# Kernel tuning notes

Hardware: AMD Instinct MI355X
Metric: run time of the kernel (lower is better)

## Reference

```python
import jax, jax.numpy as jnp
import numpy as np

B, N, D, NS, HID, ITERS = 32, 4096, 256, 8, 128, 3
EPS = 1e-8
LN_EPS = 1e-5


def _ln(x, g, b):
    mu = jnp.mean(x, axis=-1, keepdims=True)
    var = jnp.mean(jnp.square(x - mu), axis=-1, keepdims=True)
    return (x - mu) * jax.lax.rsqrt(var + LN_EPS) * g + b


def setup_inputs() -> dict:
    key = jax.random.key(0)
    ks = jax.random.split(key, 32)
    scale = D ** -0.5

    def lin(k, out_d, in_d):
        return jax.random.normal(k, (out_d, in_d), jnp.float32) * (in_d ** -0.5)

    inp = {
        "inputs": jax.random.normal(ks[0], (B, N, D), jnp.float32),
        "slot_noise": jax.random.normal(ks[1], (B, NS, D), jnp.float32),
        "slots_mu": jax.random.uniform(ks[2], (1, 1, D), jnp.float32, -1.0, 1.0) * scale,
        "slots_sigma": jax.random.uniform(ks[3], (1, 1, D), jnp.float32, -1.0, 1.0) * scale,
        "Wq": lin(ks[4], D, D),
        "Wk": lin(ks[5], D, D),
        "Wv": lin(ks[6], D, D),
        "gru_w_ih": lin(ks[7], 3 * D, 2 * D),
        "gru_w_hh": lin(ks[8], 3 * D, D),
        "gru_b_ih": jnp.zeros((3 * D,), jnp.float32),
        "gru_b_hh": jnp.zeros((3 * D,), jnp.float32),
        "obj_w1": lin(ks[9], HID, D),
        "obj_b1": jnp.zeros((HID,), jnp.float32),
        "obj_w2": lin(ks[10], D, HID),
        "obj_b2": jnp.zeros((D,), jnp.float32),
        "rel_w1": lin(ks[11], HID, 2 * D),
        "rel_b1": jnp.zeros((HID,), jnp.float32),
        "rel_w2": lin(ks[12], D, HID),
        "rel_b2": jnp.zeros((D,), jnp.float32),
        "ln_in_g": jnp.ones((D,), jnp.float32),
        "ln_in_b": jnp.zeros((D,), jnp.float32),
        "ln_s_g": jnp.ones((D,), jnp.float32),
        "ln_s_b": jnp.zeros((D,), jnp.float32),
        "ln_ff_g": jnp.ones((D,), jnp.float32),
        "ln_ff_b": jnp.zeros((D,), jnp.float32),
    }
    return inp


def _rel_msg(x, rel_w1, rel_b1, rel_w2, rel_b2):
    # x: (b, n_s, d). rel_mlp(cat(x_i, x_j)) without materializing the concat:
    # split first layer weight into the x_i and x_j halves.
    A = rel_w1[:, :D]   # (hid, d)
    Bm = rel_w1[:, D:]  # (hid, d)
    xa = jnp.einsum('bid,hd->bih', x, A)
    xb = jnp.einsum('bjd,hd->bjh', x, Bm)
    h = jax.nn.relu(xa[:, :, None, :] + xb[:, None, :, :] + rel_b1)  # (b,ns,ns,hid)
    msg = jnp.einsum('bijh,dh->bijd', h, rel_w2) + rel_b2            # (b,ns,ns,d)
    n_s = x.shape[1]
    diag = jnp.eye(n_s, dtype=bool)[None, :, :, None]
    msg = jnp.where(diag, 0.0, msg)
    return msg.sum(axis=2) / (n_s - 1)


def _gru_cell(x, h, w_ih, w_hh, b_ih, b_hh):
    gx = x @ w_ih.T + b_ih  # (B*, 3d)
    gh = h @ w_hh.T + b_hh
    xr, xz, xn = jnp.split(gx, 3, axis=-1)
    hr, hz, hn = jnp.split(gh, 3, axis=-1)
    r = jax.nn.sigmoid(xr + hr)
    z = jax.nn.sigmoid(xz + hz)
    n = jnp.tanh(xn + r * hn)
    return (1.0 - z) * n + z * h


def reference(inputs, slot_noise, slots_mu, slots_sigma, Wq, Wk, Wv,
              gru_w_ih, gru_w_hh, gru_b_ih, gru_b_hh,
              obj_w1, obj_b1, obj_w2, obj_b2,
              rel_w1, rel_b1, rel_w2, rel_b2,
              ln_in_g, ln_in_b, ln_s_g, ln_s_b, ln_ff_g, ln_ff_b):
    b, n, d = inputs.shape
    n_s = slot_noise.shape[1]
    scale = d ** -0.5

    slots = slots_mu + slot_noise * jnp.exp(slots_sigma)  # (b, n_s, d)

    x = _ln(inputs, ln_in_g, ln_in_b)
    k = jnp.einsum('bnd,ed->bne', x, Wk)
    v = jnp.einsum('bnd,ed->bne', x, Wv)

    attns = []
    for _ in range(ITERS):
        slots_prev = slots
        q = jnp.einsum('bid,ed->bie', _ln(slots, ln_s_g, ln_s_b), Wq)
        dots = jnp.einsum('bid,bjd->bij', q, k) * scale        # (b, n_s, n)
        attn = jax.nn.softmax(dots, axis=1) + EPS              # softmax over slots
        attns.append(attn)
        attn_n = attn / attn.sum(axis=-1, keepdims=True)
        updates = jnp.einsum('bjd,bij->bid', v, attn_n)        # (b, n_s, d)
        rel = _rel_msg(slots_prev, rel_w1, rel_b1, rel_w2, rel_b2)
        gin = jnp.concatenate([updates, rel], axis=-1).reshape(b * n_s, 2 * d)
        slots = _gru_cell(gin, slots_prev.reshape(b * n_s, d),
                          gru_w_ih, gru_w_hh, gru_b_ih, gru_b_hh).reshape(b, n_s, d)
        ff = _ln(slots, ln_ff_g, ln_ff_b)
        slots = slots + (jax.nn.relu(ff @ obj_w1.T + obj_b1) @ obj_w2.T + obj_b2)
    return slots, jnp.stack(attns)
```

## Files before the change

### kernel.cpp

```cpp
#include <hip/hip_runtime.h>
#include <hip/hip_bf16.h>
#include <math.h>

static constexpr int Bc   = 32;
static constexpr int Nc   = 4096;
static constexpr int Dc   = 256;
static constexpr int NSc  = 8;
static constexpr int HIDc = 128;
static constexpr int ITERSc = 3;
#define EPSf 1e-8f
#define LN_EPSf 1e-5f

typedef __attribute__((ext_vector_type(8))) short bf16x8;
typedef __attribute__((ext_vector_type(8))) unsigned short u16x8;
typedef __attribute__((ext_vector_type(4))) float f32x4;

static constexpr int W1AT = 0;
static constexpr int W1BT = 32768;
static constexpr int W2T  = 65536;
static constexpr int OW1T = 98304;
static constexpr int OW2T = 131072;
static constexpr int WQT  = 163840;
static constexpr int WHNT = 229376;
static constexpr int TW_ELEMS = 294912;

__device__ __forceinline__ float bf2f(unsigned int u) {
  return __uint_as_float((u & 0xffffu) << 16);
}

__device__ __forceinline__ unsigned short f2bfu(float f) {
  unsigned int u = __float_as_uint(f);
  unsigned int r = (u + 0x7fffu + ((u >> 16) & 1u)) >> 16;
  return (unsigned short)r;
}

__device__ __forceinline__ void bf8_to_f(uint4 r, float* o) {
  o[0] = bf2f(r.x); o[1] = bf2f(r.x >> 16);
  o[2] = bf2f(r.y); o[3] = bf2f(r.y >> 16);
  o[4] = bf2f(r.z); o[5] = bf2f(r.z >> 16);
  o[6] = bf2f(r.w); o[7] = bf2f(r.w >> 16);
}

__device__ __forceinline__ void gl_lds16(const void* g, void* l) {
  __builtin_amdgcn_global_load_lds(
      (__attribute__((address_space(1))) void*)(g),
      (__attribute__((address_space(3))) void*)(l), 16, 0, 0);
}

__device__ __forceinline__ float block_sum(float v, float* tmp) {
  #pragma unroll
  for (int o = 32; o > 0; o >>= 1) v += __shfl_down(v, o, 64);
  int lane = threadIdx.x & 63, wid = threadIdx.x >> 6;
  __syncthreads();
  if (lane == 0) tmp[wid] = v;
  __syncthreads();
  return tmp[0] + tmp[1] + tmp[2] + tmp[3];
}

__device__ __forceinline__ float sigmf(float x) { return 1.f / (1.f + expf(-x)); }

__global__ __launch_bounds__(256) void k_init_slots(const float* __restrict__ noise,
                                                    const float* __restrict__ mu,
                                                    const float* __restrict__ sigma,
                                                    float* __restrict__ slots) {
  int idx = blockIdx.x * 256 + threadIdx.x;
  int d = idx & (Dc - 1);
  slots[idx] = mu[d] + noise[idx] * expf(sigma[d]);
}

__global__ __launch_bounds__(256) void k_wcvt(const float* __restrict__ Wk,
                                              const float* __restrict__ Wv,
                                              unsigned short* __restrict__ wbuf) {
  int idx = blockIdx.x * 256 + threadIdx.x;
  int n = idx >> 8, k = idx & 255;
  float v = (n < 256) ? Wk[n * 256 + k] : Wv[(n - 256) * 256 + k];
  wbuf[idx] = f2bfu(v);
}

__global__ __launch_bounds__(256) void k_wprep(const float* __restrict__ w_ih,
                                               const float* __restrict__ w_hh,
                                               unsigned short* __restrict__ Wcat) {
  int idx = blockIdx.x * 256 + threadIdx.x;
  int o = idx / 768, c = idx - o * 768;
  float v;
  if (c < 512) v = w_ih[o * 512 + c];
  else v = (o < 512) ? w_hh[o * 256 + (c - 512)] : 0.f;
  Wcat[idx] = f2bfu(v);
}

__global__ __launch_bounds__(256) void k_tprep(const float* __restrict__ rel_w1,
                                               const float* __restrict__ rel_w2,
                                               const float* __restrict__ obj_w1,
                                               const float* __restrict__ obj_w2,
                                               const float* __restrict__ Wq,
                                               const float* __restrict__ w_hh,
                                               unsigned short* __restrict__ Tw) {
  int i = blockIdx.x * 256 + threadIdx.x;
  if (i >= TW_ELEMS) return;
  float v;
  if (i < W1BT) { int j = i - W1AT; int d = j >> 7, h = j & 127; v = rel_w1[h * 512 + d]; }
  else if (i < W2T)  { int j = i - W1BT; int d = j >> 7, h = j & 127; v = rel_w1[h * 512 + 256 + d]; }
  else if (i < OW1T) { int j = i - W2T;  int h = j >> 8, o = j & 255; v = rel_w2[o * 128 + h]; }
  else if (i < OW2T) { int j = i - OW1T; int d = j >> 7, h = j & 127; v = obj_w1[h * 256 + d]; }
  else if (i < WQT)  { int j = i - OW2T; int h = j >> 8, o = j & 255; v = obj_w2[o * 128 + h]; }
  else if (i < WHNT) { int j = i - WQT;  int d = j >> 8, e = j & 255; v = Wq[e * 256 + d]; }
  else               { int j = i - WHNT; int d = j >> 8, o = j & 255; v = w_hh[(512 + o) * 256 + d]; }
  Tw[i] = f2bfu(v);
}

__global__ __launch_bounds__(256, 2) void k_gemm_kv(const float* __restrict__ inp,
                                                    const float* __restrict__ lng,
                                                    const float* __restrict__ lnb,
                                                    const unsigned short* __restrict__ wbuf,
                                                    unsigned short* __restrict__ kbuf,
                                                    unsigned short* __restrict__ vbuf) {
  __shared__ unsigned short Als[64 * 64];
  __shared__ unsigned short Bls[512 * 64];
  __shared__ float smu[64];
  __shared__ float srs[64];
  int tid = threadIdx.x;
  int lane = tid & 63, w = tid >> 6;
  int idx16 = lane & 15, quad = lane >> 4;
  int m0 = blockIdx.x * 64;

  for (int rr = 0; rr < 16; rr++) {
    int row = w * 16 + rr;
    float4 v = *(const float4*)(inp + (size_t)(m0 + row) * 256 + lane * 4);
    float s = v.x + v.y + v.z + v.w;
    float q = v.x * v.x + v.y * v.y + v.z * v.z + v.w * v.w;
    #pragma unroll
    for (int o = 32; o > 0; o >>= 1) { s += __shfl_down(s, o, 64); q += __shfl_down(q, o, 64); }
    if (lane == 0) {
      float mu = s * (1.0f / 256.0f);
      float var = q * (1.0f / 256.0f) - mu * mu;
      smu[row] = mu;
      srs[row] = rsqrtf(var + LN_EPSf);
    }
  }
  __syncthreads();

  f32x4 acc[4][8];
  #pragma unroll
  for (int i = 0; i < 4; i++)
    #pragma unroll
    for (int j = 0; j < 8; j++) acc[i][j] = (f32x4){0.f, 0.f, 0.f, 0.f};

  for (int kt = 0; kt < 4; kt++) {
    int k0 = kt * 64;
    #pragma unroll
    for (int c = 0; c < 16; c++) {
      int idx = (w * 16 + c) * 64 + lane;
      int row = idx >> 3, lc = idx & 7;
      int gc = lc ^ (row & 7);
      gl_lds16((const char*)wbuf + ((size_t)row * 256 + k0) * 2 + gc * 16,
               (char*)Bls + (size_t)(w * 16 + c) * 1024);
    }
    #pragma unroll
    for (int p = 0; p < 2; p++) {
      int idx = p * 256 + tid;
      int row = idx >> 3, c8 = idx & 7;
      const float* src = inp + (size_t)(m0 + row) * 256 + k0 + c8 * 8;
      float mu = smu[row], rs = srs[row];
      float4 x0 = *(const float4*)(src);
      float4 x1 = *(const float4*)(src + 4);
      float4 g0 = *(const float4*)(lng + k0 + c8 * 8);
      float4 g1 = *(const float4*)(lng + k0 + c8 * 8 + 4);
      float4 b0 = *(const float4*)(lnb + k0 + c8 * 8);
      float4 b1 = *(const float4*)(lnb + k0 + c8 * 8 + 4);
      u16x8 pk;
      pk[0] = f2bfu((x0.x - mu) * rs * g0.x + b0.x);
      pk[1] = f2bfu((x0.y - mu) * rs * g0.y + b0.y);
      pk[2] = f2bfu((x0.z - mu) * rs * g0.z + b0.z);
      pk[3] = f2bfu((x0.w - mu) * rs * g0.w + b0.w);
      pk[4] = f2bfu((x1.x - mu) * rs * g1.x + b1.x);
      pk[5] = f2bfu((x1.y - mu) * rs * g1.y + b1.y);
      pk[6] = f2bfu((x1.z - mu) * rs * g1.z + b1.z);
      pk[7] = f2bfu((x1.w - mu) * rs * g1.w + b1.w);
      int dchunk = c8 ^ (row & 7);
      *(u16x8*)((char*)Als + (size_t)(row * 8 + dchunk) * 16) = pk;
    }
    __syncthreads();
    #pragma unroll
    for (int ks = 0; ks < 2; ks++) {
      int kchunk = ks * 4 + quad;
      bf16x8 af[4], bfr[8];
      #pragma unroll
      for (int mt = 0; mt < 4; mt++) {
        int row = mt * 16 + idx16;
        af[mt] = *(const bf16x8*)((const char*)Als + (size_t)(row * 8 + (kchunk ^ (row & 7))) * 16);
      }
      #pragma unroll
      for (int nt = 0; nt < 8; nt++) {
        int row = w * 128 + nt * 16 + idx16;
        bfr[nt] = *(const bf16x8*)((const char*)Bls + (size_t)(row * 8 + (kchunk ^ (row & 7))) * 16);
      }
      #pragma unroll
      for (int mt = 0; mt < 4; mt++)
        #pragma unroll
        for (int nt = 0; nt < 8; nt++)
          acc[mt][nt] = __builtin_amdgcn_mfma_f32_16x16x32_bf16(af[mt], bfr[nt], acc[mt][nt], 0, 0, 0);
    }
    __syncthreads();
  }
  #pragma unroll
  for (int mt = 0; mt < 4; mt++) {
    #pragma unroll
    for (int nt = 0; nt < 8; nt++) {
      int gm = m0 + mt * 16 + quad * 4;
      int col = w * 128 + nt * 16 + idx16;
      unsigned short* dst = (col < 256) ? kbuf : vbuf;
      int c = col & 255;
      #pragma unroll
      for (int r = 0; r < 4; r++)
        dst[(size_t)(gm + r) * 256 + c] = f2bfu(acc[mt][nt][r]);
    }
  }
}

__global__ __launch_bounds__(256) void k_qproj0(const float* __restrict__ slots,
                                                const unsigned short* __restrict__ Tw,
                                                const float* __restrict__ g,
                                                const float* __restrict__ bb_,
                                                unsigned short* __restrict__ qb,
                                                float* __restrict__ S,
                                                float* __restrict__ updraw) {
  __shared__ float xs[Dc];
  __shared__ float tmp[4];
  int t = threadIdx.x;
  int row = blockIdx.x;
  updraw[row * 256 + t] = 0.f;
  if (blockIdx.x == 0) S[t] = 0.f;
  float x = slots[row * Dc + t];
  float s = block_sum(x, tmp);
  float m = s * (1.0f / Dc);
  float dx = x - m;
  float s2 = block_sum(dx * dx, tmp);
  float rs = rsqrtf(s2 * (1.0f / Dc) + LN_EPSf);
  xs[t] = dx * rs * g[t] + bb_[t];
  __syncthreads();
  float acc = 0.f;
  const unsigned short* wq = Tw + WQT;
  for (int d = 0; d < 256; d++) acc += bf2f(wq[d * 256 + t]) * xs[d];
  qb[row * 256 + t] = f2bfu(acc);
}

__global__ __launch_bounds__(256) void k_attn(const unsigned short* __restrict__ qb,
                                              const unsigned short* __restrict__ kbuf,
                                              const unsigned short* __restrict__ vbuf,
                                              float* __restrict__ attn,
                                              float* __restrict__ S,
                                              float* __restrict__ updraw) {
  __shared__ float qs[NSc][Dc];
  __shared__ float at[NSc][256];
  __shared__ float parts[2][NSc][256];
  int t = threadIdx.x;
  int b = blockIdx.x >> 4;
  int jc = blockIdx.x & 15;
  int j0 = jc * 256;
  for (int x = t; x < NSc * Dc; x += 256) qs[x >> 8][x & 255] = bf2f(qb[b * NSc * Dc + x]);
  __syncthreads();
  int j = j0 + t;
  const uint4* krow = (const uint4*)(kbuf + ((size_t)b * Nc + j) * Dc);
  float dot[NSc];
  #pragma unroll
  for (int i = 0; i < NSc; i++) dot[i] = 0.f;
  for (int d8 = 0; d8 < Dc / 8; d8++) {
    float kv[8];
    bf8_to_f(krow[d8], kv);
    #pragma unroll
    for (int i = 0; i < NSc; i++) {
      const float* qr = &qs[i][d8 * 8];
      float s0 = 0.f;
      #pragma unroll
      for (int u = 0; u < 8; u++) s0 += kv[u] * qr[u];
      dot[i] += s0;
    }
  }
  float m = -1e30f;
  #pragma unroll
  for (int i = 0; i < NSc; i++) { float s = dot[i] * 0.0625f; dot[i] = s; m = fmaxf(m, s); }
  float sum = 0.f;
  float a[NSc];
  #pragma unroll
  for (int i = 0; i < NSc; i++) { float e = expf(dot[i] - m); a[i] = e; sum += e; }
  float inv = 1.f / sum;
  #pragma unroll
  for (int i = 0; i < NSc; i++) a[i] = a[i] * inv + EPSf;
  float* ab = attn + (size_t)b * NSc * Nc;
  #pragma unroll
  for (int i = 0; i < NSc; i++) {
    ab[i * Nc + j] = a[i];
    at[i][t] = a[i];
  }
  __syncthreads();
  {
    int wv = t >> 6, lane = t & 63;
    #pragma unroll
    for (int ii = 0; ii < 2; ii++) {
      int i = wv + ii * 4;
      float4 v = *(const float4*)&at[i][lane * 4];
      float s = v.x + v.y + v.z + v.w;
      #pragma unroll
      for (int o = 32; o > 0; o >>= 1) s += __shfl_down(s, o, 64);
      if (lane == 0) atomicAdd(&S[b * NSc + i], s);
    }
  }
  int rsh = t >> 7, dg = t & 127;
  float acc[NSc][2];
  #pragma unroll
  for (int i = 0; i < NSc; i++) { acc[i][0] = 0.f; acc[i][1] = 0.f; }
  const unsigned short* vr = vbuf + ((size_t)b * Nc + j0 + rsh * 128) * Dc + dg * 2;
  for (int jj = 0; jj < 128; jj += 2) {
    unsigned int v0 = *(const unsigned int*)(vr + (size_t)jj * Dc);
    unsigned int v1 = *(const unsigned int*)(vr + (size_t)(jj + 1) * Dc);
    float v0a = bf2f(v0), v0b = bf2f(v0 >> 16);
    float v1a = bf2f(v1), v1b = bf2f(v1 >> 16);
    #pragma unroll
    for (int i = 0; i < NSc; i++) {
      float2 ap = *(const float2*)&at[i][rsh * 128 + jj];
      acc[i][0] += ap.x * v0a + ap.y * v1a;
      acc[i][1] += ap.x * v0b + ap.y * v1b;
    }
  }
  #pragma unroll
  for (int i = 0; i < NSc; i++) {
    parts[rsh][i][dg * 2] = acc[i][0];
    parts[rsh][i][dg * 2 + 1] = acc[i][1];
  }
  __syncthreads();
  for (int i = 0; i < NSc; i++) {
    float val = parts[0][i][t] + parts[1][i][t];
    atomicAdd(&updraw[(b * NSc + i) * 256 + t], val);
  }
}

__global__ __launch_bounds__(256) void k_slot_a(const float* __restrict__ slots,
                                                const float* __restrict__ updraw,
                                                const float* __restrict__ S,
                                                const unsigned short* __restrict__ Tw,
                                                const float* __restrict__ b1,
                                                const float* __restrict__ b2,
                                                unsigned short* __restrict__ Xb) {
  __shared__ float sp[NSc][256];
  __shared__ float xpart[2][12][128];
  __shared__ float xabl[12][128];
  __shared__ float hs[4][128];
  int t = threadIdx.x;
  int b = blockIdx.x >> 1, half = blockIdx.x & 1;
  int i0 = half * 4;
  for (int x = t; x < NSc * 256; x += 256) sp[x >> 8][x & 255] = slots[b * NSc * 256 + x];
  __syncthreads();
  for (int r = 0; r < 4; r++) {
    int grow = b * NSc + i0 + r;
    float u = updraw[grow * 256 + t] / S[grow];
    Xb[(size_t)grow * 768 + t] = f2bfu(u);
    Xb[(size_t)grow * 768 + 512 + t] = f2bfu(sp[i0 + r][t]);
  }
  int h = t & 127, dh = t >> 7;
  {
    const unsigned short* wa = Tw + W1AT;
    const unsigned short* wb = Tw + W1BT;
    float accb[8] = {0, 0, 0, 0, 0, 0, 0, 0};
    float acca[4] = {0, 0, 0, 0};
    for (int dd = 0; dd < 128; dd++) {
      int d = dh * 128 + dd;
      float wbv = bf2f(wb[d * 128 + h]);
      float wav = bf2f(wa[d * 128 + h]);
      #pragma unroll
      for (int jj = 0; jj < 8; jj++) accb[jj] += wbv * sp[jj][d];
      #pragma unroll
      for (int r = 0; r < 4; r++) acca[r] += wav * sp[i0 + r][d];
    }
    #pragma unroll
    for (int jj = 0; jj < 8; jj++) xpart[dh][jj][h] = accb[jj];
    #pragma unroll
    for (int r = 0; r < 4; r++) xpart[dh][8 + r][h] = acca[r];
  }
  __syncthreads();
  {
    int g = t >> 7;
    for (int jj = g * 6; jj < g * 6 + 6; jj++)
      xabl[jj][h] = xpart[0][jj][h] + xpart[1][jj][h];
  }
  __syncthreads();
  {
    float bv = b1[h];
    int ig = t >> 7;
    #pragma unroll
    for (int ii = 0; ii < 2; ii++) {
      int il = ig * 2 + ii;
      int ibatch = i0 + il;
      float av = xabl[8 + il][h];
      float s = 0.f;
      #pragma unroll
      for (int jj = 0; jj < NSc; jj++) {
        if (jj == ibatch) continue;
        s += fmaxf(av + xabl[jj][h] + bv, 0.f);
      }
      hs[il][h] = s;
    }
  }
  __syncthreads();
  {
    const unsigned short* w2 = Tw + W2T;
    float am[4] = {0, 0, 0, 0};
    for (int hh = 0; hh < 128; hh++) {
      float wv = bf2f(w2[hh * 256 + t]);
      #pragma unroll
      for (int r = 0; r < 4; r++) am[r] += wv * hs[r][hh];
    }
    float bv2 = b2[t];
    for (int r = 0; r < 4; r++) {
      float rel = am[r] * (1.0f / 7.0f) + bv2;
      Xb[(size_t)(b * NSc + i0 + r) * 768 + 256 + t] = f2bfu(rel);
    }
  }
}

__global__ __launch_bounds__(256) void k_gates(const unsigned short* __restrict__ Xb,
                                               const unsigned short* __restrict__ Wcat,
                                               unsigned short* __restrict__ Yb) {
  __shared__ unsigned short Als[64 * 64];
  __shared__ unsigned short Bls[64 * 64];
  int tid = threadIdx.x;
  int lane = tid & 63, w = tid >> 6;
  int idx16 = lane & 15, quad = lane >> 4;
  int m0 = (blockIdx.x / 12) * 64;
  int n0 = (blockIdx.x % 12) * 64;
  int wm = w & 1, wn = w >> 1;
  f32x4 acc[2][2];
  #pragma unroll
  for (int i = 0; i < 2; i++)
    #pragma unroll
    for (int j = 0; j < 2; j++) acc[i][j] = (f32x4){0.f, 0.f, 0.f, 0.f};

  for (int kt = 0; kt < 12; kt++) {
    int k0 = kt * 64;
    #pragma unroll
    for (int c = 0; c < 2; c++) {
      int idx = (w * 2 + c) * 64 + lane;
      int row = idx >> 3, lc = idx & 7;
      int gc = lc ^ (row & 7);
      gl_lds16((const char*)Xb + (size_t)(m0 + row) * 1536 + k0 * 2 + gc * 16,
               (char*)Als + (size_t)(w * 2 + c) * 1024);
      gl_lds16((const char*)Wcat + (size_t)(n0 + row) * 1536 + k0 * 2 + gc * 16,
               (char*)Bls + (size_t)(w * 2 + c) * 1024);
    }
    __syncthreads();
    #pragma unroll
    for (int ks = 0; ks < 2; ks++) {
      bf16x8 af[2], bfr[2];
      int kchunk = ks * 4 + quad;
      #pragma unroll
      for (int mt = 0; mt < 2; mt++) {
        int row = wm * 32 + mt * 16 + idx16;
        af[mt] = *(const bf16x8*)((const char*)Als + (size_t)(row * 8 + (kchunk ^ (row & 7))) * 16);
      }
      #pragma unroll
      for (int nt = 0; nt < 2; nt++) {
        int row = wn * 32 + nt * 16 + idx16;
        bfr[nt] = *(const bf16x8*)((const char*)Bls + (size_t)(row * 8 + (kchunk ^ (row & 7))) * 16);
      }
      #pragma unroll
      for (int mt = 0; mt < 2; mt++)
        #pragma unroll
        for (int nt = 0; nt < 2; nt++)
          acc[mt][nt] = __builtin_amdgcn_mfma_f32_16x16x32_bf16(af[mt], bfr[nt], acc[mt][nt], 0, 0, 0);
    }
    __syncthreads();
  }
  #pragma unroll
  for (int mt = 0; mt < 2; mt++) {
    #pragma unroll
    for (int nt = 0; nt < 2; nt++) {
      int gm = m0 + wm * 32 + mt * 16 + quad * 4;
      int col = n0 + wn * 32 + nt * 16 + idx16;
      #pragma unroll
      for (int r = 0; r < 4; r++)
        Yb[(size_t)(gm + r) * 768 + col] = f2bfu(acc[mt][nt][r]);
    }
  }
}

__global__ __launch_bounds__(256) void k_slot_c(const unsigned short* __restrict__ Yb,
                                                const unsigned short* __restrict__ Tw,
                                                const float* __restrict__ b_ih,
                                                const float* __restrict__ b_hh,
                                                float* __restrict__ slots,
                                                const float* __restrict__ ob1,
                                                const float* __restrict__ ob2,
                                                const float* __restrict__ lng,
                                                const float* __restrict__ lnb,
                                                const float* __restrict__ lsg,
                                                const float* __restrict__ lsb,
                                                unsigned short* __restrict__ qb,
                                                float* __restrict__ updraw,
                                                float* __restrict__ S,
                                                float* __restrict__ outf,
                                                int wfinal) {
  __shared__ float sp4[4][256];
  __shared__ float ffl[4][256];
  __shared__ float h1p[2][4][128];
  __shared__ float h1l[4][128];
  __shared__ float xs2[4][256];
  int t = threadIdx.x;
  int g0 = blockIdx.x * 4;
  for (int x = t; x < 1024; x += 256) sp4[x >> 8][x & 255] = slots[(size_t)g0 * 256 + x];
  __syncthreads();
  float hn[4] = {0, 0, 0, 0};
  {
    const unsigned short* wh = Tw + WHNT;
    for (int d = 0; d < 256; d++) {
      float wv = bf2f(wh[d * 256 + t]);
      #pragma unroll
      for (int r = 0; r < 4; r++) hn[r] += wv * sp4[r][d];
    }
  }
  float bir = b_ih[t], bhr = b_hh[t];
  float biz = b_ih[256 + t], bhz = b_hh[256 + t];
  float bin_ = b_ih[512 + t], bhn = b_hh[512 + t];
  float snew[4];
  #pragma unroll
  for (int r = 0; r < 4; r++) {
    size_t yoff = (size_t)(g0 + r) * 768;
    float yr = bf2f((unsigned int)Yb[yoff + t]);
    float yz = bf2f((unsigned int)Yb[yoff + 256 + t]);
    float yx = bf2f((unsigned int)Yb[yoff + 512 + t]);
    float rg = sigmf(yr + bir + bhr);
    float zg = sigmf(yz + biz + bhz);
    float ng = tanhf(yx + bin_ + rg * (hn[r] + bhn));
    snew[r] = (1.f - zg) * ng + zg * sp4[r][t];
    ffl[r][t] = snew[r];
  }
  __syncthreads();
  {
    int wv = t >> 6, lane = t & 63;
    float4 v = *(const float4*)&ffl[wv][lane * 4];
    float s = v.x + v.y + v.z + v.w;
    float q = v.x * v.x + v.y * v.y + v.z * v.z + v.w * v.w;
    #pragma unroll
    for (int o = 32; o > 0; o >>= 1) { s += __shfl_down(s, o, 64); q += __shfl_down(q, o, 64); }
    s = __shfl(s, 0, 64); q = __shfl(q, 0, 64);
    float mu = s * (1.0f / 256.0f);
    float rs = rsqrtf(q * (1.0f / 256.0f) - mu * mu + LN_EPSf);
    float4 g4 = *(const float4*)&lng[lane * 4];
    float4 b4 = *(const float4*)&lnb[lane * 4];
    float4 o4;
    o4.x = (v.x - mu) * rs * g4.x + b4.x;
    o4.y = (v.y - mu) * rs * g4.y + b4.y;
    o4.z = (v.z - mu) * rs * g4.z + b4.z;
    o4.w = (v.w - mu) * rs * g4.w + b4.w;
    *(float4*)&ffl[wv][lane * 4] = o4;
  }
  __syncthreads();
  {
    const unsigned short* w1 = Tw + OW1T;
    int h = t & 127, dh = t >> 7;
    float a1[4] = {0, 0, 0, 0};
    for (int dd = 0; dd < 128; dd++) {
      int d = dh * 128 + dd;
      float wv = bf2f(w1[d * 128 + h]);
      #pragma unroll
      for (int r = 0; r < 4; r++) a1[r] += wv * ffl[r][d];
    }
    #pragma unroll
    for (int r = 0; r < 4; r++) h1p[dh][r][h] = a1[r];
  }
  __syncthreads();
  {
    int h = t & 127, g = t >> 7;
    float bo = ob1[h];
    #pragma unroll
    for (int rr = 0; rr < 2; rr++) {
      int r = g * 2 + rr;
      h1l[r][h] = fmaxf(h1p[0][r][h] + h1p[1][r][h] + bo, 0.f);
    }
  }
  __syncthreads();
  float res[4];
  {
    const unsigned short* w2 = Tw + OW2T;
    float ao[4] = {0, 0, 0, 0};
    for (int hh = 0; hh < 128; hh++) {
      float wv = bf2f(w2[hh * 256 + t]);
      #pragma unroll
      for (int r = 0; r < 4; r++) ao[r] += wv * h1l[r][hh];
    }
    float bo2 = ob2[t];
    #pragma unroll
    for (int r = 0; r < 4; r++) res[r] = snew[r] + ao[r] + bo2;
  }
  #pragma unroll
  for (int r = 0; r < 4; r++) {
    slots[(size_t)(g0 + r) * 256 + t] = res[r];
    if (wfinal) outf[(size_t)(g0 + r) * 256 + t] = res[r];
    xs2[r][t] = res[r];
  }
  __syncthreads();
  {
    int wv = t >> 6, lane = t & 63;
    float4 v = *(const float4*)&xs2[wv][lane * 4];
    float s = v.x + v.y + v.z + v.w;
    float q = v.x * v.x + v.y * v.y + v.z * v.z + v.w * v.w;
    #pragma unroll
    for (int o = 32; o > 0; o >>= 1) { s += __shfl_down(s, o, 64); q += __shfl_down(q, o, 64); }
    s = __shfl(s, 0, 64); q = __shfl(q, 0, 64);
    float mu = s * (1.0f / 256.0f);
    float rs = rsqrtf(q * (1.0f / 256.0f) - mu * mu + LN_EPSf);
    float4 g4 = *(const float4*)&lsg[lane * 4];
    float4 b4 = *(const float4*)&lsb[lane * 4];
    float4 o4;
    o4.x = (v.x - mu) * rs * g4.x + b4.x;
    o4.y = (v.y - mu) * rs * g4.y + b4.y;
    o4.z = (v.z - mu) * rs * g4.z + b4.z;
    o4.w = (v.w - mu) * rs * g4.w + b4.w;
    *(float4*)&xs2[wv][lane * 4] = o4;
  }
  __syncthreads();
  {
    const unsigned short* wq = Tw + WQT;
    float aq[4] = {0, 0, 0, 0};
    for (int d = 0; d < 256; d++) {
      float wv = bf2f(wq[d * 256 + t]);
      #pragma unroll
      for (int r = 0; r < 4; r++) aq[r] += wv * xs2[r][d];
    }
    #pragma unroll
    for (int r = 0; r < 4; r++) qb[(size_t)(g0 + r) * 256 + t] = f2bfu(aq[r]);
  }
  #pragma unroll
  for (int r = 0; r < 4; r++) updraw[(size_t)(g0 + r) * 256 + t] = 0.f;
  if (t < 4) S[g0 + t] = 0.f;
}

extern "C" void kernel_launch(void* const* d_in, const int* in_sizes, int n_in,
                              void* d_out, int out_size, void* d_ws, size_t ws_size,
                              hipStream_t stream) {
  const float* inputs      = (const float*)d_in[0];
  const float* slot_noise  = (const float*)d_in[1];
  const float* slots_mu    = (const float*)d_in[2];
  const float* slots_sigma = (const float*)d_in[3];
  const float* Wq          = (const float*)d_in[4];
  const float* Wk          = (const float*)d_in[5];
  const float* Wv          = (const float*)d_in[6];
  const float* gru_w_ih    = (const float*)d_in[7];
  const float* gru_w_hh    = (const float*)d_in[8];
  const float* gru_b_ih    = (const float*)d_in[9];
  const float* gru_b_hh    = (const float*)d_in[10];
  const float* obj_w1      = (const float*)d_in[11];
  const float* obj_b1      = (const float*)d_in[12];
  const float* obj_w2      = (const float*)d_in[13];
  const float* obj_b2      = (const float*)d_in[14];
  const float* rel_w1      = (const float*)d_in[15];
  const float* rel_b1      = (const float*)d_in[16];
  const float* rel_w2      = (const float*)d_in[17];
  const float* rel_b2      = (const float*)d_in[18];
  const float* ln_in_g     = (const float*)d_in[19];
  const float* ln_in_b     = (const float*)d_in[20];
  const float* ln_s_g      = (const float*)d_in[21];
  const float* ln_s_b      = (const float*)d_in[22];
  const float* ln_ff_g     = (const float*)d_in[23];
  const float* ln_ff_b     = (const float*)d_in[24];

  char* w = (char*)d_ws;
  unsigned short* kbuf = (unsigned short*)(w);
  unsigned short* vbuf = (unsigned short*)(w + (size_t)67108864);
  float* slots  = (float*)(w + (size_t)134217728);
  float* updraw = (float*)(w + (size_t)134479872);
  float* Sbuf   = (float*)(w + (size_t)134742016);
  unsigned short* Wcat = (unsigned short*)(w + (size_t)134743040);
  unsigned short* Tw   = (unsigned short*)(w + (size_t)135922688);
  unsigned short* Xbuf = (unsigned short*)(w + (size_t)136512512);
  unsigned short* qb   = (unsigned short*)(w + (size_t)136512512);
  unsigned short* Ybuf = (unsigned short*)(w + (size_t)136905728);
  unsigned short* wbuf = (unsigned short*)(w + (size_t)136905728);

  float* out = (float*)d_out;
  float* attn_base = out + (size_t)Bc * NSc * Dc;

  k_init_slots<<<Bc * NSc * Dc / 256, 256, 0, stream>>>(slot_noise, slots_mu, slots_sigma, slots);
  k_wcvt<<<512, 256, 0, stream>>>(Wk, Wv, wbuf);
  k_wprep<<<768 * 768 / 256, 256, 0, stream>>>(gru_w_ih, gru_w_hh, Wcat);
  k_tprep<<<(TW_ELEMS + 255) / 256, 256, 0, stream>>>(rel_w1, rel_w2, obj_w1, obj_w2, Wq, gru_w_hh, Tw);
  k_gemm_kv<<<Bc * Nc / 64, 256, 0, stream>>>(inputs, ln_in_g, ln_in_b, wbuf, kbuf, vbuf);
  k_qproj0<<<Bc * NSc, 256, 0, stream>>>(slots, Tw, ln_s_g, ln_s_b, qb, Sbuf, updraw);

  for (int it = 0; it < ITERSc; it++) {
    float* attn = attn_base + (size_t)it * Bc * NSc * Nc;
    k_attn<<<Bc * 16, 256, 0, stream>>>(qb, kbuf, vbuf, attn, Sbuf, updraw);
    k_slot_a<<<Bc * 2, 256, 0, stream>>>(slots, updraw, Sbuf, Tw, rel_b1, rel_b2, Xbuf);
    k_gates<<<4 * 12, 256, 0, stream>>>(Xbuf, Wcat, Ybuf);
    k_slot_c<<<64, 256, 0, stream>>>(Ybuf, Tw, gru_b_ih, gru_b_hh, slots,
                                     obj_b1, obj_b2, ln_ff_g, ln_ff_b, ln_s_g, ln_s_b,
                                     qb, updraw, Sbuf,
                                     out, it == ITERSc - 1 ? 1 : 0);
  }
}
```

Baseline: 692.5 us.

## Fold Wk into query and Wv after attention to drop K/V projection GEMM

The full K and V projections over all tokens are removed. Queries are premultiplied by Wq^T·Wk (precomputed as MT), so attention logits come straight from the layer-normed inputs X stored once in bf16. The attention-weighted sum is taken over X, and Wv is applied afterwards to the small per-slot result in k_slot_a. This replaces a large GEMM and two 64MB buffers with one 64MB normalized-input buffer. Dots now use a 16x16 MFMA with half the rows zero-padded. Rounding changes, since MT is fp32 but X is bf16.

```diff
diff --git a/kernel.cpp b/kernel.cpp
--- a/kernel.cpp
+++ b/kernel.cpp
@@ -20,9 +20,8 @@
 static constexpr int W2T  = 65536;
 static constexpr int OW1T = 98304;
 static constexpr int OW2T = 131072;
-static constexpr int WQT  = 163840;
-static constexpr int WHNT = 229376;
-static constexpr int TW_ELEMS = 294912;
+static constexpr int WHNT = 163840;
+static constexpr int TW_ELEMS = 229376;
 
 __device__ __forceinline__ float bf2f(unsigned int u) {
   return __uint_as_float((u & 0xffffu) << 16);
@@ -32,13 +31,6 @@
   unsigned int u = __float_as_uint(f);
   unsigned int r = (u + 0x7fffu + ((u >> 16) & 1u)) >> 16;
   return (unsigned short)r;
-}
-
-__device__ __forceinline__ void bf8_to_f(uint4 r, float* o) {
-  o[0] = bf2f(r.x); o[1] = bf2f(r.x >> 16);
-  o[2] = bf2f(r.y); o[3] = bf2f(r.y >> 16);
-  o[4] = bf2f(r.z); o[5] = bf2f(r.z >> 16);
-  o[6] = bf2f(r.w); o[7] = bf2f(r.w >> 16);
 }
 
 __device__ __forceinline__ void gl_lds16(const void* g, void* l) {
@@ -68,13 +60,50 @@
   slots[idx] = mu[d] + noise[idx] * expf(sigma[d]);
 }
 
-__global__ __launch_bounds__(256) void k_wcvt(const float* __restrict__ Wk,
-                                              const float* __restrict__ Wv,
-                                              unsigned short* __restrict__ wbuf) {
-  int idx = blockIdx.x * 256 + threadIdx.x;
-  int n = idx >> 8, k = idx & 255;
-  float v = (n < 256) ? Wk[n * 256 + k] : Wv[(n - 256) * 256 + k];
-  wbuf[idx] = f2bfu(v);
+__global__ __launch_bounds__(256) void k_lnx(const float* __restrict__ inp,
+                                             const float* __restrict__ lng,
+                                             const float* __restrict__ lnb,
+                                             unsigned short* __restrict__ X) {
+  __shared__ float smu[16], srs[16];
+  int t = threadIdx.x, lane = t & 63, w = t >> 6;
+  size_t row0 = (size_t)blockIdx.x * 16;
+  for (int rr = 0; rr < 4; rr++) {
+    int row = w * 4 + rr;
+    float4 v = *(const float4*)(inp + (row0 + row) * 256 + lane * 4);
+    float s = v.x + v.y + v.z + v.w;
+    float q = v.x * v.x + v.y * v.y + v.z * v.z + v.w * v.w;
+    #pragma unroll
+    for (int o = 32; o > 0; o >>= 1) { s += __shfl_down(s, o, 64); q += __shfl_down(q, o, 64); }
+    if (lane == 0) {
+      float mu = s * (1.0f / 256.0f);
+      smu[row] = mu;
+      srs[row] = rsqrtf(q * (1.0f / 256.0f) - mu * mu + LN_EPSf);
+    }
+  }
+  __syncthreads();
+  #pragma unroll
+  for (int p = 0; p < 2; p++) {
+    int idx = p * 256 + t;
+    int row = idx >> 5, ch = idx & 31;
+    const float* src = inp + (row0 + row) * 256 + ch * 8;
+    float mu = smu[row], rs = srs[row];
+    float4 x0 = *(const float4*)(src);
+    float4 x1 = *(const float4*)(src + 4);
+    float4 g0 = *(const float4*)(lng + ch * 8);
+    float4 g1 = *(const float4*)(lng + ch * 8 + 4);
+    float4 b0 = *(const float4*)(lnb + ch * 8);
+    float4 b1 = *(const float4*)(lnb + ch * 8 + 4);
+    u16x8 pk;
+    pk[0] = f2bfu((x0.x - mu) * rs * g0.x + b0.x);
+    pk[1] = f2bfu((x0.y - mu) * rs * g0.y + b0.y);
+    pk[2] = f2bfu((x0.z - mu) * rs * g0.z + b0.z);
+    pk[3] = f2bfu((x0.w - mu) * rs * g0.w + b0.w);
+    pk[4] = f2bfu((x1.x - mu) * rs * g1.x + b1.x);
+    pk[5] = f2bfu((x1.y - mu) * rs * g1.y + b1.y);
+    pk[6] = f2bfu((x1.z - mu) * rs * g1.z + b1.z);
+    pk[7] = f2bfu((x1.w - mu) * rs * g1.w + b1.w);
+    *(u16x8*)(X + (row0 + row) * 256 + ch * 8) = pk;
+  }
 }
 
 __global__ __launch_bounds__(256) void k_wprep(const float* __restrict__ w_ih,
@@ -92,7 +121,6 @@
                                                const float* __restrict__ rel_w2,
                                                const float* __restrict__ obj_w1,
                                                const float* __restrict__ obj_w2,
-                                               const float* __restrict__ Wq,
                                                const float* __restrict__ w_hh,
                                                unsigned short* __restrict__ Tw) {
   int i = blockIdx.x * 256 + threadIdx.x;
@@ -102,126 +130,28 @@
   else if (i < W2T)  { int j = i - W1BT; int d = j >> 7, h = j & 127; v = rel_w1[h * 512 + 256 + d]; }
   else if (i < OW1T) { int j = i - W2T;  int h = j >> 8, o = j & 255; v = rel_w2[o * 128 + h]; }
   else if (i < OW2T) { int j = i - OW1T; int d = j >> 7, h = j & 127; v = obj_w1[h * 256 + d]; }
-  else if (i < WQT)  { int j = i - OW2T; int h = j >> 8, o = j & 255; v = obj_w2[o * 128 + h]; }
-  else if (i < WHNT) { int j = i - WQT;  int d = j >> 8, e = j & 255; v = Wq[e * 256 + d]; }
+  else if (i < WHNT) { int j = i - OW2T; int h = j >> 8, o = j & 255; v = obj_w2[o * 128 + h]; }
   else               { int j = i - WHNT; int d = j >> 8, o = j & 255; v = w_hh[(512 + o) * 256 + d]; }
   Tw[i] = f2bfu(v);
 }
 
-__global__ __launch_bounds__(256, 2) void k_gemm_kv(const float* __restrict__ inp,
-                                                    const float* __restrict__ lng,
-                                                    const float* __restrict__ lnb,
-                                                    const unsigned short* __restrict__ wbuf,
-                                                    unsigned short* __restrict__ kbuf,
-                                                    unsigned short* __restrict__ vbuf) {
-  __shared__ unsigned short Als[64 * 64];
-  __shared__ unsigned short Bls[512 * 64];
-  __shared__ float smu[64];
-  __shared__ float srs[64];
-  int tid = threadIdx.x;
-  int lane = tid & 63, w = tid >> 6;
-  int idx16 = lane & 15, quad = lane >> 4;
-  int m0 = blockIdx.x * 64;
-
-  for (int rr = 0; rr < 16; rr++) {
-    int row = w * 16 + rr;
-    float4 v = *(const float4*)(inp + (size_t)(m0 + row) * 256 + lane * 4);
-    float s = v.x + v.y + v.z + v.w;
-    float q = v.x * v.x + v.y * v.y + v.z * v.z + v.w * v.w;
-    #pragma unroll
-    for (int o = 32; o > 0; o >>= 1) { s += __shfl_down(s, o, 64); q += __shfl_down(q, o, 64); }
-    if (lane == 0) {
-      float mu = s * (1.0f / 256.0f);
-      float var = q * (1.0f / 256.0f) - mu * mu;
-      smu[row] = mu;
-      srs[row] = rsqrtf(var + LN_EPSf);
-    }
-  }
-  __syncthreads();
-
-  f32x4 acc[4][8];
-  #pragma unroll
-  for (int i = 0; i < 4; i++)
-    #pragma unroll
-    for (int j = 0; j < 8; j++) acc[i][j] = (f32x4){0.f, 0.f, 0.f, 0.f};
-
-  for (int kt = 0; kt < 4; kt++) {
-    int k0 = kt * 64;
-    #pragma unroll
-    for (int c = 0; c < 16; c++) {
-      int idx = (w * 16 + c) * 64 + lane;
-      int row = idx >> 3, lc = idx & 7;
-      int gc = lc ^ (row & 7);
-      gl_lds16((const char*)wbuf + ((size_t)row * 256 + k0) * 2 + gc * 16,
-               (char*)Bls + (size_t)(w * 16 + c) * 1024);
-    }
-    #pragma unroll
-    for (int p = 0; p < 2; p++) {
-      int idx = p * 256 + tid;
-      int row = idx >> 3, c8 = idx & 7;
-      const float* src = inp + (size_t)(m0 + row) * 256 + k0 + c8 * 8;
-      float mu = smu[row], rs = srs[row];
-      float4 x0 = *(const float4*)(src);
-      float4 x1 = *(const float4*)(src + 4);
-      float4 g0 = *(const float4*)(lng + k0 + c8 * 8);
-      float4 g1 = *(const float4*)(lng + k0 + c8 * 8 + 4);
-      float4 b0 = *(const float4*)(lnb + k0 + c8 * 8);
-      float4 b1 = *(const float4*)(lnb + k0 + c8 * 8 + 4);
-      u16x8 pk;
-      pk[0] = f2bfu((x0.x - mu) * rs * g0.x + b0.x);
-      pk[1] = f2bfu((x0.y - mu) * rs * g0.y + b0.y);
-      pk[2] = f2bfu((x0.z - mu) * rs * g0.z + b0.z);
-      pk[3] = f2bfu((x0.w - mu) * rs * g0.w + b0.w);
-      pk[4] = f2bfu((x1.x - mu) * rs * g1.x + b1.x);
-      pk[5] = f2bfu((x1.y - mu) * rs * g1.y + b1.y);
-      pk[6] = f2bfu((x1.z - mu) * rs * g1.z + b1.z);
-      pk[7] = f2bfu((x1.w - mu) * rs * g1.w + b1.w);
-      int dchunk = c8 ^ (row & 7);
-      *(u16x8*)((char*)Als + (size_t)(row * 8 + dchunk) * 16) = pk;
-    }
-    __syncthreads();
-    #pragma unroll
-    for (int ks = 0; ks < 2; ks++) {
-      int kchunk = ks * 4 + quad;
-      bf16x8 af[4], bfr[8];
-      #pragma unroll
-      for (int mt = 0; mt < 4; mt++) {
-        int row = mt * 16 + idx16;
-        af[mt] = *(const bf16x8*)((const char*)Als + (size_t)(row * 8 + (kchunk ^ (row & 7))) * 16);
-      }
-      #pragma unroll
-      for (int nt = 0; nt < 8; nt++) {
-        int row = w * 128 + nt * 16 + idx16;
-        bfr[nt] = *(const bf16x8*)((const char*)Bls + (size_t)(row * 8 + (kchunk ^ (row & 7))) * 16);
-      }
-      #pragma unroll
-      for (int mt = 0; mt < 4; mt++)
-        #pragma unroll
-        for (int nt = 0; nt < 8; nt++)
-          acc[mt][nt] = __builtin_amdgcn_mfma_f32_16x16x32_bf16(af[mt], bfr[nt], acc[mt][nt], 0, 0, 0);
-    }
-    __syncthreads();
-  }
-  #pragma unroll
-  for (int mt = 0; mt < 4; mt++) {
-    #pragma unroll
-    for (int nt = 0; nt < 8; nt++) {
-      int gm = m0 + mt * 16 + quad * 4;
-      int col = w * 128 + nt * 16 + idx16;
-      unsigned short* dst = (col < 256) ? kbuf : vbuf;
-      int c = col & 255;
-      #pragma unroll
-      for (int r = 0; r < 4; r++)
-        dst[(size_t)(gm + r) * 256 + c] = f2bfu(acc[mt][nt][r]);
-    }
-  }
+__global__ __launch_bounds__(256) void k_mprep(const float* __restrict__ Wk,
+                                               const float* __restrict__ Wq,
+                                               const float* __restrict__ Wv,
+                                               float* __restrict__ MT,
+                                               float* __restrict__ WvT) {
+  int d = blockIdx.x, t = threadIdx.x;
+  float acc = 0.f;
+  for (int c = 0; c < 256; c++) acc += Wk[c * 256 + t] * Wq[c * 256 + d];
+  MT[d * 256 + t] = acc;
+  WvT[d * 256 + t] = Wv[t * 256 + d];
 }
 
 __global__ __launch_bounds__(256) void k_qproj0(const float* __restrict__ slots,
-                                                const unsigned short* __restrict__ Tw,
+                                                const float* __restrict__ MT,
                                                 const float* __restrict__ g,
                                                 const float* __restrict__ bb_,
-                                                unsigned short* __restrict__ qb,
+                                                unsigned short* __restrict__ qkb,
                                                 float* __restrict__ S,
                                                 float* __restrict__ updraw) {
   __shared__ float xs[Dc];
@@ -239,98 +169,97 @@
   xs[t] = dx * rs * g[t] + bb_[t];
   __syncthreads();
   float acc = 0.f;
-  const unsigned short* wq = Tw + WQT;
-  for (int d = 0; d < 256; d++) acc += bf2f(wq[d * 256 + t]) * xs[d];
-  qb[row * 256 + t] = f2bfu(acc);
-}
-
-__global__ __launch_bounds__(256) void k_attn(const unsigned short* __restrict__ qb,
-                                              const unsigned short* __restrict__ kbuf,
-                                              const unsigned short* __restrict__ vbuf,
+  for (int d = 0; d < 256; d++) acc += MT[d * 256 + t] * xs[d];
+  int b = row >> 3, i = row & 7;
+  qkb[(size_t)(b * 16 + i) * 256 + t] = f2bfu(acc);
+  qkb[(size_t)(b * 16 + 8 + i) * 256 + t] = 0;
+}
+
+__global__ __launch_bounds__(256) void k_attn(const unsigned short* __restrict__ qkb,
+                                              const unsigned short* __restrict__ X,
                                               float* __restrict__ attn,
                                               float* __restrict__ S,
                                               float* __restrict__ updraw) {
-  __shared__ float qs[NSc][Dc];
-  __shared__ float at[NSc][256];
-  __shared__ float parts[2][NSc][256];
-  int t = threadIdx.x;
-  int b = blockIdx.x >> 4;
-  int jc = blockIdx.x & 15;
-  int j0 = jc * 256;
-  for (int x = t; x < NSc * Dc; x += 256) qs[x >> 8][x & 255] = bf2f(qb[b * NSc * Dc + x]);
-  __syncthreads();
-  int j = j0 + t;
-  const uint4* krow = (const uint4*)(kbuf + ((size_t)b * Nc + j) * Dc);
-  float dot[NSc];
-  #pragma unroll
-  for (int i = 0; i < NSc; i++) dot[i] = 0.f;
-  for (int d8 = 0; d8 < Dc / 8; d8++) {
-    float kv[8];
-    bf8_to_f(krow[d8], kv);
-    #pragma unroll
-    for (int i = 0; i < NSc; i++) {
-      const float* qr = &qs[i][d8 * 8];
-      float s0 = 0.f;
-      #pragma unroll
-      for (int u = 0; u < 8; u++) s0 += kv[u] * qr[u];
-      dot[i] += s0;
-    }
-  }
-  float m = -1e30f;
-  #pragma unroll
-  for (int i = 0; i < NSc; i++) { float s = dot[i] * 0.0625f; dot[i] = s; m = fmaxf(m, s); }
-  float sum = 0.f;
-  float a[NSc];
-  #pragma unroll
-  for (int i = 0; i < NSc; i++) { float e = expf(dot[i] - m); a[i] = e; sum += e; }
-  float inv = 1.f / sum;
-  #pragma unroll
-  for (int i = 0; i < NSc; i++) a[i] = a[i] * inv + EPSf;
-  float* ab = attn + (size_t)b * NSc * Nc;
-  #pragma unroll
-  for (int i = 0; i < NSc; i++) {
-    ab[i * Nc + j] = a[i];
-    at[i][t] = a[i];
-  }
-  __syncthreads();
-  {
-    int wv = t >> 6, lane = t & 63;
-    #pragma unroll
-    for (int ii = 0; ii < 2; ii++) {
-      int i = wv + ii * 4;
-      float4 v = *(const float4*)&at[i][lane * 4];
-      float s = v.x + v.y + v.z + v.w;
+  __shared__ unsigned short xs[64 * 256];
+  __shared__ float dots[16][68];
+  __shared__ float at[8][64];
+  __shared__ float parts[2][8][256];
+  int t = threadIdx.x, lane = t & 63, w = t >> 6;
+  int b = blockIdx.x >> 6, jc = blockIdx.x & 63;
+  int j0 = jc * 64;
+  #pragma unroll
+  for (int c = 0; c < 8; c++) {
+    int slot = c * 256 + t;
+    int tok = slot >> 5, sl = slot & 31;
+    int gc = (sl & 24) | ((sl & 7) ^ (tok & 7));
+    gl_lds16((const char*)X + (((size_t)(b * 4096 + j0 + tok)) * 256 + gc * 8) * 2,
+             (char*)xs + (size_t)(c * 256 + w * 64) * 16);
+  }
+  int m = lane & 15, quad = lane >> 4;
+  const unsigned short* qrow = qkb + (size_t)(b * 16 + m) * 256;
+  __syncthreads();
+  f32x4 dacc = {0.f, 0.f, 0.f, 0.f};
+  int tokb = w * 16 + m;
+  #pragma unroll
+  for (int ks = 0; ks < 8; ks++) {
+    bf16x8 afr = *(const bf16x8*)(qrow + ks * 32 + quad * 8);
+    int kchunk = ks * 4 + quad;
+    int slot = (kchunk & 24) | ((kchunk & 7) ^ (tokb & 7));
+    bf16x8 bfr = *(const bf16x8*)((const char*)xs + (size_t)tokb * 512 + slot * 16);
+    dacc = __builtin_amdgcn_mfma_f32_16x16x32_bf16(afr, bfr, dacc, 0, 0, 0);
+  }
+  #pragma unroll
+  for (int r = 0; r < 4; r++) dots[quad * 4 + r][tokb] = dacc[r];
+  __syncthreads();
+  if (t < 64) {
+    float a[8], mx = -1e30f;
+    #pragma unroll
+    for (int i = 0; i < 8; i++) { a[i] = dots[i][t] * 0.0625f; mx = fmaxf(mx, a[i]); }
+    float sum = 0.f;
+    #pragma unroll
+    for (int i = 0; i < 8; i++) { a[i] = expf(a[i] - mx); sum += a[i]; }
+    float inv = 1.f / sum;
+    float* ab = attn + (size_t)b * NSc * Nc;
+    #pragma unroll
+    for (int i = 0; i < 8; i++) {
+      float v = a[i] * inv + EPSf;
+      a[i] = v;
+      at[i][t] = v;
+      ab[i * Nc + j0 + t] = v;
+    }
+    #pragma unroll
+    for (int i = 0; i < 8; i++) {
+      float s = a[i];
       #pragma unroll
       for (int o = 32; o > 0; o >>= 1) s += __shfl_down(s, o, 64);
       if (lane == 0) atomicAdd(&S[b * NSc + i], s);
     }
   }
-  int rsh = t >> 7, dg = t & 127;
-  float acc[NSc][2];
-  #pragma unroll
-  for (int i = 0; i < NSc; i++) { acc[i][0] = 0.f; acc[i][1] = 0.f; }
-  const unsigned short* vr = vbuf + ((size_t)b * Nc + j0 + rsh * 128) * Dc + dg * 2;
-  for (int jj = 0; jj < 128; jj += 2) {
-    unsigned int v0 = *(const unsigned int*)(vr + (size_t)jj * Dc);
-    unsigned int v1 = *(const unsigned int*)(vr + (size_t)(jj + 1) * Dc);
-    float v0a = bf2f(v0), v0b = bf2f(v0 >> 16);
-    float v1a = bf2f(v1), v1b = bf2f(v1 >> 16);
-    #pragma unroll
-    for (int i = 0; i < NSc; i++) {
-      float2 ap = *(const float2*)&at[i][rsh * 128 + jj];
-      acc[i][0] += ap.x * v0a + ap.y * v1a;
-      acc[i][1] += ap.x * v0b + ap.y * v1b;
-    }
-  }
-  #pragma unroll
-  for (int i = 0; i < NSc; i++) {
-    parts[rsh][i][dg * 2] = acc[i][0];
-    parts[rsh][i][dg * 2 + 1] = acc[i][1];
-  }
-  __syncthreads();
-  for (int i = 0; i < NSc; i++) {
+  __syncthreads();
+  int dg = t & 127, h = t >> 7;
+  float acc[8][2];
+  #pragma unroll
+  for (int i = 0; i < 8; i++) { acc[i][0] = 0.f; acc[i][1] = 0.f; }
+  int kchunk = dg >> 2;
+  for (int jj = 0; jj < 32; jj++) {
+    int tok = h * 32 + jj;
+    int slot = (kchunk & 24) | ((kchunk & 7) ^ (tok & 7));
+    unsigned int xv = *(const unsigned int*)((const char*)xs + (size_t)tok * 512 + slot * 16 + (dg & 3) * 4);
+    float x0 = bf2f(xv), x1 = bf2f(xv >> 16);
+    #pragma unroll
+    for (int i = 0; i < 8; i++) {
+      float av = at[i][tok];
+      acc[i][0] += av * x0;
+      acc[i][1] += av * x1;
+    }
+  }
+  #pragma unroll
+  for (int i = 0; i < 8; i++)
+    *(float2*)&parts[h][i][dg * 2] = make_float2(acc[i][0], acc[i][1]);
+  __syncthreads();
+  for (int i = 0; i < 8; i++) {
     float val = parts[0][i][t] + parts[1][i][t];
-    atomicAdd(&updraw[(b * NSc + i) * 256 + t], val);
+    atomicAdd(&updraw[(size_t)(b * NSc + i) * 256 + t], val);
   }
 }
 
@@ -338,10 +267,12 @@
                                                 const float* __restrict__ updraw,
                                                 const float* __restrict__ S,
                                                 const unsigned short* __restrict__ Tw,
+                                                const float* __restrict__ WvT,
                                                 const float* __restrict__ b1,
                                                 const float* __restrict__ b2,
                                                 unsigned short* __restrict__ Xb) {
   __shared__ float sp[NSc][256];
+  __shared__ float un[4][256];
   __shared__ float xpart[2][12][128];
   __shared__ float xabl[12][128];
   __shared__ float hs[4][128];
@@ -349,12 +280,23 @@
   int b = blockIdx.x >> 1, half = blockIdx.x & 1;
   int i0 = half * 4;
   for (int x = t; x < NSc * 256; x += 256) sp[x >> 8][x & 255] = slots[b * NSc * 256 + x];
-  __syncthreads();
   for (int r = 0; r < 4; r++) {
     int grow = b * NSc + i0 + r;
-    float u = updraw[grow * 256 + t] / S[grow];
-    Xb[(size_t)grow * 768 + t] = f2bfu(u);
-    Xb[(size_t)grow * 768 + 512 + t] = f2bfu(sp[i0 + r][t]);
+    un[r][t] = updraw[(size_t)grow * 256 + t] / S[grow];
+  }
+  __syncthreads();
+  {
+    float av[4] = {0.f, 0.f, 0.f, 0.f};
+    for (int d = 0; d < 256; d++) {
+      float wv = WvT[d * 256 + t];
+      #pragma unroll
+      for (int r = 0; r < 4; r++) av[r] += wv * un[r][d];
+    }
+    for (int r = 0; r < 4; r++) {
+      int grow = b * NSc + i0 + r;
+      Xb[(size_t)grow * 768 + t] = f2bfu(av[r]);
+      Xb[(size_t)grow * 768 + 512 + t] = f2bfu(sp[i0 + r][t]);
+    }
   }
   int h = t & 127, dh = t >> 7;
   {
@@ -484,6 +426,7 @@
 
 __global__ __launch_bounds__(256) void k_slot_c(const unsigned short* __restrict__ Yb,
                                                 const unsigned short* __restrict__ Tw,
+                                                const float* __restrict__ MT,
                                                 const float* __restrict__ b_ih,
                                                 const float* __restrict__ b_hh,
                                                 float* __restrict__ slots,
@@ -493,7 +436,7 @@
                                                 const float* __restrict__ lnb,
                                                 const float* __restrict__ lsg,
                                                 const float* __restrict__ lsb,
-                                                unsigned short* __restrict__ qb,
+                                                unsigned short* __restrict__ qkb,
                                                 float* __restrict__ updraw,
                                                 float* __restrict__ S,
                                                 float* __restrict__ outf,
@@ -618,15 +561,19 @@
   }
   __syncthreads();
   {
-    const unsigned short* wq = Tw + WQT;
     float aq[4] = {0, 0, 0, 0};
     for (int d = 0; d < 256; d++) {
-      float wv = bf2f(wq[d * 256 + t]);
+      float wv = MT[d * 256 + t];
       #pragma unroll
       for (int r = 0; r < 4; r++) aq[r] += wv * xs2[r][d];
     }
     #pragma unroll
-    for (int r = 0; r < 4; r++) qb[(size_t)(g0 + r) * 256 + t] = f2bfu(aq[r]);
+    for (int r = 0; r < 4; r++) {
+      int grow = g0 + r;
+      int b = grow >> 3, i = grow & 7;
+      qkb[(size_t)(b * 16 + i) * 256 + t] = f2bfu(aq[r]);
+      qkb[(size_t)(b * 16 + 8 + i) * 256 + t] = 0;
+    }
   }
   #pragma unroll
   for (int r = 0; r < 4; r++) updraw[(size_t)(g0 + r) * 256 + t] = 0.f;
@@ -663,36 +610,36 @@
   const float* ln_ff_b     = (const float*)d_in[24];
 
   char* w = (char*)d_ws;
-  unsigned short* kbuf = (unsigned short*)(w);
-  unsigned short* vbuf = (unsigned short*)(w + (size_t)67108864);
-  float* slots  = (float*)(w + (size_t)134217728);
-  float* updraw = (float*)(w + (size_t)134479872);
-  float* Sbuf   = (float*)(w + (size_t)134742016);
-  unsigned short* Wcat = (unsigned short*)(w + (size_t)134743040);
-  unsigned short* Tw   = (unsigned short*)(w + (size_t)135922688);
-  unsigned short* Xbuf = (unsigned short*)(w + (size_t)136512512);
-  unsigned short* qb   = (unsigned short*)(w + (size_t)136512512);
-  unsigned short* Ybuf = (unsigned short*)(w + (size_t)136905728);
-  unsigned short* wbuf = (unsigned short*)(w + (size_t)136905728);
+  unsigned short* X    = (unsigned short*)(w);
+  float* slots  = (float*)(w + (size_t)67108864);
+  float* updraw = (float*)(w + (size_t)67371008);
+  float* Sbuf   = (float*)(w + (size_t)67633152);
+  unsigned short* Wcat = (unsigned short*)(w + (size_t)67634176);
+  unsigned short* Tw   = (unsigned short*)(w + (size_t)68813824);
+  unsigned short* Xbuf = (unsigned short*)(w + (size_t)69403648);
+  unsigned short* Ybuf = (unsigned short*)(w + (size_t)69796864);
+  unsigned short* qkb  = (unsigned short*)(w + (size_t)70190080);
+  float* MT  = (float*)(w + (size_t)70452224);
+  float* WvT = (float*)(w + (size_t)70714368);
 
   float* out = (float*)d_out;
   float* attn_base = out + (size_t)Bc * NSc * Dc;
 
   k_init_slots<<<Bc * NSc * Dc / 256, 256, 0, stream>>>(slot_noise, slots_mu, slots_sigma, slots);
-  k_wcvt<<<512, 256, 0, stream>>>(Wk, Wv, wbuf);
+  k_lnx<<<Bc * Nc / 16, 256, 0, stream>>>(inputs, ln_in_g, ln_in_b, X);
   k_wprep<<<768 * 768 / 256, 256, 0, stream>>>(gru_w_ih, gru_w_hh, Wcat);
-  k_tprep<<<(TW_ELEMS + 255) / 256, 256, 0, stream>>>(rel_w1, rel_w2, obj_w1, obj_w2, Wq, gru_w_hh, Tw);
-  k_gemm_kv<<<Bc * Nc / 64, 256, 0, stream>>>(inputs, ln_in_g, ln_in_b, wbuf, kbuf, vbuf);
-  k_qproj0<<<Bc * NSc, 256, 0, stream>>>(slots, Tw, ln_s_g, ln_s_b, qb, Sbuf, updraw);
+  k_tprep<<<(TW_ELEMS + 255) / 256, 256, 0, stream>>>(rel_w1, rel_w2, obj_w1, obj_w2, gru_w_hh, Tw);
+  k_mprep<<<256, 256, 0, stream>>>(Wk, Wq, Wv, MT, WvT);
+  k_qproj0<<<Bc * NSc, 256, 0, stream>>>(slots, MT, ln_s_g, ln_s_b, qkb, Sbuf, updraw);
 
   for (int it = 0; it < ITERSc; it++) {
     float* attn = attn_base + (size_t)it * Bc * NSc * Nc;
-    k_attn<<<Bc * 16, 256, 0, stream>>>(qb, kbuf, vbuf, attn, Sbuf, updraw);
-    k_slot_a<<<Bc * 2, 256, 0, stream>>>(slots, updraw, Sbuf, Tw, rel_b1, rel_b2, Xbuf);
+    k_attn<<<Bc * 64, 256, 0, stream>>>(qkb, X, attn, Sbuf, updraw);
+    k_slot_a<<<Bc * 2, 256, 0, stream>>>(slots, updraw, Sbuf, Tw, WvT, rel_b1, rel_b2, Xbuf);
     k_gates<<<4 * 12, 256, 0, stream>>>(Xbuf, Wcat, Ybuf);
-    k_slot_c<<<64, 256, 0, stream>>>(Ybuf, Tw, gru_b_ih, gru_b_hh, slots,
+    k_slot_c<<<64, 256, 0, stream>>>(Ybuf, Tw, MT, gru_b_ih, gru_b_hh, slots,
                                      obj_b1, obj_b2, ln_ff_g, ln_ff_b, ln_s_g, ln_s_b,
-                                     qb, updraw, Sbuf,
+                                     qkb, updraw, Sbuf,
                                      out, it == ITERSc - 1 ? 1 : 0);
   }
 }
```

After: 798.3 us. 1.15x slower.
